# Kernel tuning notes

Measured on AMD Instinct MI355X. Metric: run time of the kernel, lower is better.

## Reference

```python
import jax, jax.numpy as jnp
import numpy as np

D_MODEL = 192
D_INNER = 384          # expand(2) * d_model
HEADDIM = 12
NHEADS = 32            # d_inner // headdim
DSTATE = 16
NGROUPS = 1
CONV_DIM = D_INNER + 2 * NGROUPS * DSTATE          # 416
D_IN_PROJ = 2 * D_INNER + 2 * NGROUPS * DSTATE + NHEADS  # 832
LN_EPS = 1e-5


def silu(x):
    return x * jax.nn.sigmoid(x)


def depthwise_conv2d(x_nchw, w, b):
    # groups == channels depthwise conv, kernel 3, padding 1 (SAME)
    out = jax.lax.conv_general_dilated(
        x_nchw, w, window_strides=(1, 1), padding='SAME',
        feature_group_count=CONV_DIM,
        dimension_numbers=('NCHW', 'OIHW', 'NCHW'))
    return out + b[None, :, None, None]


def setup_inputs() -> dict:
    key = jax.random.key(0)
    ks = jax.random.split(key, 10)
    Bn, H, W = 4, 128, 128
    u = jax.random.normal(ks[0], (Bn, H, W, D_MODEL), jnp.float32)
    t = jax.random.normal(ks[1], (Bn, H, W, D_MODEL), jnp.float32)
    s_in = 1.0 / np.sqrt(D_MODEL)
    W_in = jax.random.normal(ks[2], (D_IN_PROJ, D_MODEL), jnp.float32) * s_in
    W_t_in = jax.random.normal(ks[3], (D_IN_PROJ, D_MODEL), jnp.float32) * s_in
    conv_w = jax.random.normal(ks[4], (CONV_DIM, 1, 3, 3), jnp.float32) * (1.0 / 3.0)
    conv_b = jnp.zeros((CONV_DIM,), jnp.float32)
    # dt_bias = inverse-softplus of dt sampled log-uniform in [dt_min, dt_max]
    dt0 = jnp.exp(jax.random.uniform(ks[5], (NHEADS,)) * (np.log(0.1) - np.log(0.001)) + np.log(0.001))
    dt_bias = dt0 + jnp.log(-jnp.expm1(-dt0))
    A_log = jnp.log(jax.random.uniform(ks[6], (NHEADS,), minval=1.0, maxval=16.0))
    D = jnp.ones((NHEADS,), jnp.float32)
    ln_gamma = jnp.ones((D_INNER,), jnp.float32)
    ln_beta = jnp.zeros((D_INNER,), jnp.float32)
    W_out = jax.random.normal(ks[7], (D_MODEL, D_INNER), jnp.float32) * (1.0 / np.sqrt(D_INNER))
    return dict(u=u, t=t, W_in=W_in, W_t_in=W_t_in, conv_w=conv_w, conv_b=conv_b,
                dt_bias=dt_bias, A_log=A_log, D=D, ln_gamma=ln_gamma, ln_beta=ln_beta,
                W_out=W_out)


def reference(u, t, W_in, W_t_in, conv_w, conv_b, dt_bias, A_log, D,
              ln_gamma, ln_beta, W_out):
    B0, H, W_, C0 = u.shape
    L = H * W_
    uu = u.reshape(B0, L, C0)
    tt = t.reshape(B0, L, C0)

    # in_proj on main branch: split into z, xBC, dt
    zxbcdt = uu @ W_in.T                                    # (B, L, 832)
    z = zxbcdt[..., :D_INNER]                               # (B, L, 384)
    xBC = zxbcdt[..., D_INNER:D_INNER + CONV_DIM]           # (B, L, 416)
    dt = zxbcdt[..., D_INNER + CONV_DIM:]                   # (B, L, 32)
    dt = jax.nn.softplus(dt + dt_bias)

    # t branch: only x1B1C1 part is ultimately used (C := C1)
    x1B1C1 = (tt @ W_t_in.T)[..., D_INNER:D_INNER + CONV_DIM]

    # depthwise 3x3 conv + silu on both branches
    xBC = xBC.reshape(B0, H, W_, CONV_DIM).transpose(0, 3, 1, 2)
    xBC = silu(depthwise_conv2d(xBC, conv_w, conv_b))
    xBC = xBC.transpose(0, 2, 3, 1).reshape(B0, L, CONV_DIM)

    x1B1C1 = x1B1C1.reshape(B0, H, W_, CONV_DIM).transpose(0, 3, 1, 2)
    x1B1C1 = silu(depthwise_conv2d(x1B1C1, conv_w, conv_b))
    x1B1C1 = x1B1C1.transpose(0, 2, 3, 1).reshape(B0, L, CONV_DIM)

    x = xBC[..., :D_INNER]                                  # V features (B, L, 384)
    Bk = xBC[..., D_INNER:D_INNER + NGROUPS * DSTATE]       # K (B, L, 16)
    Cq = x1B1C1[..., D_INNER + NGROUPS * DSTATE:]           # Q from t-branch (B, L, 16)

    A = -jnp.exp(A_log)                                     # (nheads,), negative

    # non-causal linear attention duality (ngroups == 1)
    V = x.reshape(B0, L, NHEADS, HEADDIM).transpose(0, 2, 1, 3)   # (B, h, L, d)
    dtT = dt.transpose(0, 2, 1)                                   # (B, h, L)
    dA = -(dtT[..., None] * A[None, :, None, None])               # ssd_positve_dA: positive
    V_scaled = V * dA
    KV = jnp.einsum('bln,bhld->bhnd', Bk, V_scaled)               # (B, h, 16, 12)
    y = jnp.einsum('bln,bhnd->bhld', Cq, KV) + V * D[None, :, None, None]
    y = y.transpose(0, 2, 1, 3).reshape(B0, L, D_INNER)

    # LayerNorm over d_inner
    mu = jnp.mean(y, axis=-1, keepdims=True)
    var = jnp.mean((y - mu) ** 2, axis=-1, keepdims=True)
    y = (y - mu) * jax.lax.rsqrt(var + LN_EPS) * ln_gamma + ln_beta

    y = y * z
    out = y @ W_out.T
    return out.reshape(B0, H, W_, C0)
```

## Files before the change

### kernel.cpp

```cpp
#include <hip/hip_runtime.h>
#include <hip/hip_bf16.h>
#include <math.h>


#define BN 4
#define HH 128
#define WWID 128
#define LTOK (HH*WWID)
#define NTOK (BN*LTOK)
#define DMODEL 192
#define DINNER 384
#define NH 32
#define HD 12
#define DST 16
#define CONVD 416
#define KVCHUNKS 64
#define PM 256
#define TILE_SH 12288
#define TILE_BY 24576
#define TROW ((size_t)NTOK*64)
#define YPAD 392

typedef __hip_bfloat16 bf16;
typedef unsigned int uint32;
typedef unsigned short ushort16;
typedef __attribute__((ext_vector_type(8))) short bf16x8;
typedef __attribute__((ext_vector_type(4))) float f32x4;
typedef __attribute__((ext_vector_type(16))) float f32x16;

__device__ __forceinline__ float bflo(uint32 v){ return __uint_as_float((v & 0xffffu) << 16); }
__device__ __forceinline__ float bfhi(uint32 v){ return __uint_as_float(v & 0xffff0000u); }
__device__ __forceinline__ ushort16 f2bf(float f){
    __hip_bfloat16 h = __float2bfloat16(f);
    return *reinterpret_cast<const ushort16*>(&h);
}
__device__ __forceinline__ float ldbf(const bf16* p){
    return __uint_as_float(((uint32)(*(const ushort16*)p)) << 16);
}
__device__ __forceinline__ float ldbfs(const short* p){
    return __uint_as_float(((uint32)(ushort16)(*p)) << 16);
}
__device__ __forceinline__ float softplusf(float x){
    return (x > 20.f) ? x : log1pf(expf(x));
}
__device__ __forceinline__ float siluf(float x){
    return x / (1.f + expf(-x));
}

union BFPK { short s[8]; bf16x8 v; };

__global__ __launch_bounds__(256) void k_prep(
    const float* __restrict__ Win, const float* __restrict__ Wout,
    const float* __restrict__ cw,
    bf16* __restrict__ Wsw, bf16* __restrict__ Wout_sh, float* __restrict__ wtr)
{
    const int i = blockIdx.x*256 + threadIdx.x;
    if (i < 832*DMODEL) {
        const int ch = i / DMODEL, k = i - ch*DMODEL;
        const int nt = ch >> 6, row = ch & 63;
        const int ks = k ^ ((row & 7) << 3);
        Wsw[(size_t)nt*TILE_SH + row*DMODEL + ks] = __float2bfloat16(Win[i]);
    }
    if (i < DMODEL*DINNER) {
        const int m = i / DINNER, k = i - m*DINNER;
        const int ni = m >> 4, mr = m & 15;
        const int ks = k >> 5, kq = (k >> 3) & 3, ii = k & 7;
        const int lane = kq*16 + mr;
        Wout_sh[(size_t)((ni*12 + ks)*64 + lane)*8 + ii] = __float2bfloat16(Wout[i]);
    }
    if (i < CONVD*9) { const int c = i/9, k = i - c*9; wtr[k*420 + c] = cw[i]; }
}

__global__ __launch_bounds__(512) void k_proj_mfma(
    const float* __restrict__ u, const bf16* __restrict__ Wsw,
    const float* __restrict__ dt_b, const float* __restrict__ A_log,
    bf16* __restrict__ z_bf, bf16* __restrict__ xbc_pre, float* __restrict__ dA)
{
    __shared__ __align__(16) short S[3*TILE_SH];

    const int tid = threadIdx.x;
    const int m0 = blockIdx.x * PM;
    const int ntbase = blockIdx.y * 7;
    const int ntiles = blockIdx.y ? 6 : 7;
    const int wid = tid >> 6, lane = tid & 63;
    const int fr = lane & 31;
    const int hi = lane >> 5;

    const char* gW = (const char*)Wsw;
    auto GLOAD = [&](int nt, int buf) {
        const char* src = gW + (size_t)nt*TILE_BY + wid*3072 + lane*16;
        char* dst = ((char*)S) + buf*TILE_BY + wid*3072;
        #pragma unroll
        for (int c = 0; c < 3; ++c)
            __builtin_amdgcn_global_load_lds(
                (const __attribute__((address_space(1))) void*)(src + c*1024),
                (__attribute__((address_space(3))) void*)(dst + c*1024), 16, 0, 0);
    };

    GLOAD(ntbase, 0);

    const float db = dt_b[fr];
    const float al = expf(A_log[fr]);
    bf16x8 a[12];
    {
        const float* arow = u + (size_t)(m0 + wid*32 + fr)*DMODEL;
        #pragma unroll
        for (int ks=0;ks<12;++ks) {
            const float4 a0 = *(const float4*)(arow + ks*16 + hi*8);
            const float4 a1 = *(const float4*)(arow + ks*16 + hi*8 + 4);
            BFPK pk;
            pk.s[0]=(short)f2bf(a0.x); pk.s[1]=(short)f2bf(a0.y);
            pk.s[2]=(short)f2bf(a0.z); pk.s[3]=(short)f2bf(a0.w);
            pk.s[4]=(short)f2bf(a1.x); pk.s[5]=(short)f2bf(a1.y);
            pk.s[6]=(short)f2bf(a1.z); pk.s[7]=(short)f2bf(a1.w);
            a[ks] = pk.v;
        }
    }
    asm volatile("s_waitcnt vmcnt(0)" ::: "memory");
    GLOAD(ntbase + 1, 1);
    __builtin_amdgcn_s_barrier();
    __builtin_amdgcn_sched_barrier(0);

    const int kswz = (fr & 7) << 3;

    for (int i = 0; i < ntiles; ++i) {
        const int nt = ntbase + i;
        const short* Sb = &S[(i % 3)*TILE_SH];

        f32x16 acc0, acc1;
        #pragma unroll
        for (int q=0;q<16;++q) { acc0[q]=0.f; acc1[q]=0.f; }

        #pragma unroll
        for (int ks=0;ks<12;++ks) {
            const int kk = (ks*16 + hi*8) ^ kswz;
            const bf16x8 b0 = *(const bf16x8*)&Sb[fr*DMODEL + kk];
            const bf16x8 b1 = *(const bf16x8*)&Sb[(32+fr)*DMODEL + kk];
            acc0 = __builtin_amdgcn_mfma_f32_32x32x16_bf16(a[ks], b0, acc0, 0, 0, 0);
            acc1 = __builtin_amdgcn_mfma_f32_32x32x16_bf16(a[ks], b1, acc1, 0, 0, 0);
        }

        #pragma unroll
        for (int ni=0;ni<2;++ni) {
            const f32x16& ac = ni ? acc1 : acc0;
            const int n0 = nt*64 + ni*32;
            if (n0 < DINNER) {
                bf16* dst = z_bf + (size_t)nt*TROW + (ni*32 + fr);
                #pragma unroll
                for (int r=0;r<16;++r) {
                    const int tok = m0 + wid*32 + (r&3) + 8*(r>>2) + 4*hi;
                    dst[(size_t)tok*64] = __float2bfloat16(ac[r]);
                }
            } else if (n0 < 800) {
                const int loc = n0 - DINNER + fr;
                bf16* dst = xbc_pre + (size_t)(loc>>6)*TROW + (loc & 63);
                #pragma unroll
                for (int r=0;r<16;++r) {
                    const int tok = m0 + wid*32 + (r&3) + 8*(r>>2) + 4*hi;
                    dst[(size_t)tok*64] = __float2bfloat16(ac[r]);
                }
            } else {
                #pragma unroll
                for (int r=0;r<16;++r) {
                    const int tok = m0 + wid*32 + (r&3) + 8*(r>>2) + 4*hi;
                    const float dt = softplusf(ac[r] + db);
                    dA[(size_t)tok*NH + fr] = dt * al;
                }
            }
        }

        if (i + 2 < ntiles) {
            GLOAD(nt + 2, (i + 2) % 3);
            asm volatile("s_waitcnt vmcnt(35)" ::: "memory");
        } else {
            asm volatile("s_waitcnt vmcnt(32)" ::: "memory");
        }
        __builtin_amdgcn_s_barrier();
        __builtin_amdgcn_sched_barrier(0);
    }
}

__global__ __launch_bounds__(256) void k_tproj(
    const float* __restrict__ t, const float* __restrict__ Wtin, float* __restrict__ cq_pre)
{
    __shared__ float ts[16][196];
    __shared__ float ws[16][196];
    const int tid = threadIdx.x;
    const int tok0 = blockIdx.x * 16;
    #pragma unroll
    for (int i = 0; i < 3; ++i) {
        const int flat = tid + 256*i;
        const int row = flat / 48, c = (flat % 48)*4;
        *(float4*)&ts[row][c] = *(const float4*)(t    + (size_t)(tok0+row)*DMODEL + c);
        *(float4*)&ws[row][c] = *(const float4*)(Wtin + (size_t)(784+row)*DMODEL + c);
    }
    __syncthreads();
    const int tt = tid >> 4, n = tid & 15;
    float s0=0.f,s1=0.f,s2=0.f,s3=0.f;
    #pragma unroll 4
    for (int k = 0; k < DMODEL; k += 4) {
        s0 = fmaf(ts[tt][k+0], ws[n][k+0], s0);
        s1 = fmaf(ts[tt][k+1], ws[n][k+1], s1);
        s2 = fmaf(ts[tt][k+2], ws[n][k+2], s2);
        s3 = fmaf(ts[tt][k+3], ws[n][k+3], s3);
    }
    cq_pre[(size_t)(tok0+tt)*DST + n] = (s0+s1)+(s2+s3);
}

__global__ __launch_bounds__(416) void k_conv416(
    const bf16* __restrict__ in, const float* __restrict__ wtr, const float* __restrict__ cb,
    bf16* __restrict__ out)
{
    __shared__ float ws[9*420];
    __shared__ float bs[416];
    const int tid = threadIdx.x;
    for (int i = tid; i < 9*420; i += 416) ws[i] = wtr[i];
    if (tid < 416) bs[tid] = cb[tid];
    __syncthreads();

    const int pl  = tid / 52;
    const int grp = tid - pl*52;
    const int c0  = grp*8;
    const int pix = blockIdx.x*8 + pl;
    const int hw  = pix & (LTOK-1);
    const int h = hw >> 7, w = hw & 127;
    const int bb = pix >> 14;

    const bf16* inT = in + (size_t)(c0 >> 6)*TROW + (c0 & 63);

    float acc[8];
    {
        const float4 b0 = *(const float4*)&bs[c0];
        const float4 b1 = *(const float4*)&bs[c0+4];
        acc[0]=b0.x; acc[1]=b0.y; acc[2]=b0.z; acc[3]=b0.w;
        acc[4]=b1.x; acc[5]=b1.y; acc[6]=b1.z; acc[7]=b1.w;
    }

    #pragma unroll
    for (int dh=-1; dh<=1; ++dh) {
        const int hh = h + dh;
        if ((unsigned)hh >= (unsigned)HH) continue;
        #pragma unroll
        for (int dw=-1; dw<=1; ++dw) {
            const int w2 = w + dw;
            if ((unsigned)w2 >= (unsigned)WWID) continue;
            const int wi = (dh+1)*3 + (dw+1);
            const int pix2 = (bb<<14) + (hh<<7) + w2;
            const uint4 v = *(const uint4*)((const ushort16*)inT + (size_t)pix2*64);
            const float4 w0 = *(const float4*)&ws[wi*420 + c0];
            const float4 w1 = *(const float4*)&ws[wi*420 + c0 + 4];
            acc[0] = fmaf(bflo(v.x), w0.x, acc[0]);
            acc[1] = fmaf(bfhi(v.x), w0.y, acc[1]);
            acc[2] = fmaf(bflo(v.y), w0.z, acc[2]);
            acc[3] = fmaf(bfhi(v.y), w0.w, acc[3]);
            acc[4] = fmaf(bflo(v.z), w1.x, acc[4]);
            acc[5] = fmaf(bfhi(v.z), w1.y, acc[5]);
            acc[6] = fmaf(bflo(v.w), w1.z, acc[6]);
            acc[7] = fmaf(bfhi(v.w), w1.w, acc[7]);
        }
    }

    uint4 o;
    o.x = ((uint32)f2bf(siluf(acc[1])) << 16) | (uint32)f2bf(siluf(acc[0]));
    o.y = ((uint32)f2bf(siluf(acc[3])) << 16) | (uint32)f2bf(siluf(acc[2]));
    o.z = ((uint32)f2bf(siluf(acc[5])) << 16) | (uint32)f2bf(siluf(acc[4]));
    o.w = ((uint32)f2bf(siluf(acc[7])) << 16) | (uint32)f2bf(siluf(acc[6]));
    *(uint4*)((ushort16*)out + (size_t)pix*CONVD + c0) = o;
}

__global__ __launch_bounds__(256) void k_conv16(
    const float* __restrict__ in, const float* __restrict__ cw, const float* __restrict__ cb,
    bf16* __restrict__ out)
{
    const int idx = blockIdx.x*256 + threadIdx.x;
    const int cc = idx & 15;
    const int pix = idx >> 4;
    const int hw = pix & (LTOK-1);
    const int h = hw >> 7, w = hw & 127;
    const int bb = pix >> 14;
    const int c = 400 + cc;

    float wg[9];
    #pragma unroll
    for (int k=0;k<9;++k) wg[k] = cw[c*9+k];
    float a = cb[c];
    #pragma unroll
    for (int dh=-1; dh<=1; ++dh) {
        const int hh = h + dh;
        if ((unsigned)hh >= (unsigned)HH) continue;
        #pragma unroll
        for (int dw=-1; dw<=1; ++dw) {
            const int w2 = w + dw;
            if ((unsigned)w2 >= (unsigned)WWID) continue;
            a = fmaf(in[((size_t)((bb<<14)+(hh<<7)+w2))*16 + cc], wg[(dh+1)*3 + (dw+1)], a);
        }
    }
    out[(size_t)pix*16 + cc] = __float2bfloat16(siluf(a));
}

__global__ __launch_bounds__(512) void k_kv(
    const bf16* __restrict__ xbc_post, const float* __restrict__ dA,
    float* __restrict__ partial)
{
    __shared__ short vsb[16][408];
    __shared__ float das[16][32];
    const int tid = threadIdx.x;
    const int b = blockIdx.y;
    const int n = tid & 15;
    const int g = tid >> 4;

    float acc[12];
    #pragma unroll
    for (int j=0;j<12;++j) acc[j]=0.f;

    const int l0base = b*LTOK + blockIdx.x*256;

    for (int it = 0; it < 16; ++it) {
        const int l0 = l0base + it*16;
        for (int i = tid; i < 16*200; i += 512) {
            const int tok = i / 200;
            const int c2 = i - tok*200;
            const uint32 v = *(const uint32*)((const ushort16*)xbc_post
                                + (size_t)(l0+tok)*CONVD + c2*2);
            *(uint32*)&vsb[tok][c2*2] = v;
        }
        {
            const int tok = tid >> 5, h = tid & 31;
            das[tok][h] = dA[(size_t)(l0+tok)*NH + h];
        }
        __syncthreads();

        #pragma unroll
        for (int tok = 0; tok < 16; ++tok) {
            const uint32 bkraw = (uint32)(ushort16)vsb[tok][DINNER + n];
            const float s = __uint_as_float(bkraw << 16) * das[tok][g];
            const uint32* vp = (const uint32*)&vsb[tok][g*12];
            const uint32 w0 = vp[0], w1 = vp[1], w2 = vp[2];
            acc[0]  = fmaf(s, bflo(w0), acc[0]);
            acc[1]  = fmaf(s, bfhi(w0), acc[1]);
            acc[2]  = fmaf(s, bflo(w1), acc[2]);
            acc[3]  = fmaf(s, bfhi(w1), acc[3]);
            acc[4]  = fmaf(s, bflo(w2), acc[4]);
            acc[5]  = fmaf(s, bfhi(w2), acc[5]);
            const uint32* vq = (const uint32*)&vsb[tok][g*12 + 6];
            const uint32 w3 = vq[0], w4 = vq[1], w5 = vq[2];
            acc[6]  = fmaf(s, bflo(w3), acc[6]);
            acc[7]  = fmaf(s, bfhi(w3), acc[7]);
            acc[8]  = fmaf(s, bflo(w4), acc[8]);
            acc[9]  = fmaf(s, bfhi(w4), acc[9]);
            acc[10] = fmaf(s, bflo(w5), acc[10]);
            acc[11] = fmaf(s, bfhi(w5), acc[11]);
        }
        __syncthreads();
    }

    float* dst = partial + ((size_t)(b*KVCHUNKS + blockIdx.x))*6144 + (size_t)tid*12;
    #pragma unroll
    for (int j4=0;j4<3;++j4)
        *(float4*)(dst + j4*4) = make_float4(acc[j4*4], acc[j4*4+1], acc[j4*4+2], acc[j4*4+3]);
}

__global__ __launch_bounds__(256) void k_kvred(
    const float* __restrict__ partial, bf16* __restrict__ kvhl)
{
    const int idx = blockIdx.x*256 + threadIdx.x;
    const int b = idx / 6144;
    const int rem = idx - b*6144;
    const int hd = rem >> 4, n = rem & 15;
    const int h = hd / HD, d = hd - h*HD;
    const float* p = partial + (size_t)(b*KVCHUNKS)*6144 + h*192 + n*12 + d;
    float s = 0.f;
    #pragma unroll 4
    for (int c = 0; c < KVCHUNKS; ++c) s += p[(size_t)c*6144];
    const bf16 hi = __float2bfloat16(s);
    const float hif = ldbf(&hi);
    kvhl[((size_t)b*2 + 0)*6144 + rem] = hi;
    kvhl[((size_t)b*2 + 1)*6144 + rem] = __float2bfloat16(s - hif);
}

__global__ __launch_bounds__(256) void k_ynorm_out(
    const bf16* __restrict__ xbc_post, const bf16* __restrict__ cq_bf,
    const bf16* __restrict__ z_bf, const bf16* __restrict__ kvhl,
    const float* __restrict__ Dv, const float* __restrict__ ln_g, const float* __restrict__ ln_b,
    const bf16* __restrict__ Wout_sh, float* __restrict__ out)
{
    __shared__ __align__(16) short kvb[24*64*8];
    __shared__ __align__(16) short yzs[64*YPAD];
    __shared__ float gs[DINNER], bs2[DINNER], ds[DINNER];
    const int tid = threadIdx.x;
    const int token0 = blockIdx.x * 64;
    const int b = token0 >> 14;

    #pragma unroll
    for (int it = 0; it < 6; ++it) {
        const int f = tid + 256*it;
        const int t = f >> 6, l = f & 63;
        const int q = l >> 4;
        const short* src = (const short*)kvhl + ((size_t)b*2 + (q >> 1))*6144
                           + (t*16 + (l & 15))*16 + (q & 1)*8;
        *(uint4*)&kvb[(size_t)f*8] = *(const uint4*)src;
    }

    {
        const int row = tid >> 2, seg = tid & 3;
        const short* src = (const short*)xbc_post + (size_t)(token0+row)*CONVD + seg*96;
        short* dst = &yzs[row*YPAD + seg*96];
        #pragma unroll
        for (int j = 0; j < 12; ++j)
            *(uint4*)(dst + j*8) = *(const uint4*)(src + j*8);
    }

    for (int i = tid; i < DINNER; i += 256) {
        gs[i]  = ln_g[i];
        bs2[i] = ln_b[i];
        ds[i]  = Dv[i/HD];
    }
    __syncthreads();

    const int wid = tid >> 6, lane = tid & 63;
    const int fr = lane & 15, fq = lane >> 4;
    const int tokA = token0 + wid*16;

    const bf16x8 cqf = *(const bf16x8*)((const short*)cq_bf + (size_t)(tokA+fr)*DST + (fq&1)*8);

    f32x4 acc[24];
    #pragma unroll
    for (int t = 0; t < 24; ++t) {
        const bf16x8 bfv = *(const bf16x8*)&kvb[(t*64 + lane)*8];
        f32x4 z4 = (f32x4){0.f,0.f,0.f,0.f};
        acc[t] = __builtin_amdgcn_mfma_f32_16x16x32_bf16(cqf, bfv, z4, 0, 0, 0);
    }

    const int rloc0 = wid*16 + fq*4;
    const int tokj0 = tokA + fq*4;
    float s[4]  = {0.f,0.f,0.f,0.f};
    float s2[4] = {0.f,0.f,0.f,0.f};
    #pragma unroll
    for (int t = 0; t < 24; ++t) {
        const int hd = t*16 + fr;
        const float dvh = ds[hd];
        #pragma unroll
        for (int j = 0; j < 4; ++j) {
            const float vv = ldbfs(&yzs[(rloc0+j)*YPAD + hd]);
            const float y = fmaf(vv, dvh, acc[t][j]);
            acc[t][j] = y;
            s[j] += y;
            s2[j] = fmaf(y, y, s2[j]);
        }
    }
    #pragma unroll
    for (int j = 0; j < 4; ++j) {
        #pragma unroll
        for (int off = 8; off > 0; off >>= 1) {
            s[j]  += __shfl_xor(s[j],  off, 16);
            s2[j] += __shfl_xor(s2[j], off, 16);
        }
    }
    float mu[4], rs[4];
    #pragma unroll
    for (int j = 0; j < 4; ++j) {
        mu[j] = s[j] * (1.f/384.f);
        const float var = s2[j]*(1.f/384.f) - mu[j]*mu[j];
        rs[j] = rsqrtf(var + 1e-5f);
    }

    #pragma unroll
    for (int t = 0; t < 24; ++t) {
        const int hd = t*16 + fr;
        const float g = gs[hd], be = bs2[hd];
        const bf16* zsrc = z_bf + (size_t)(hd>>6)*TROW + (hd & 63);
        #pragma unroll
        for (int j = 0; j < 4; ++j) {
            const int tok = tokj0 + j;
            const float yn = fmaf((acc[t][j] - mu[j])*rs[j], g, be);
            const float zv = ldbf(zsrc + (size_t)tok*64);
            yzs[(rloc0+j)*YPAD + hd] = (short)f2bf(yn*zv);
        }
    }

    const short* yrow = &yzs[(wid*16 + fr)*YPAD];
    bf16x8 af[12];
    #pragma unroll
    for (int ks = 0; ks < 12; ++ks)
        af[ks] = *(const bf16x8*)(yrow + ks*32 + fq*8);

    f32x4 oacc[12];
    #pragma unroll
    for (int ni = 0; ni < 12; ++ni) oacc[ni] = (f32x4){0.f,0.f,0.f,0.f};

    #pragma unroll
    for (int ks = 0; ks < 12; ++ks) {
        #pragma unroll
        for (int ni = 0; ni < 12; ++ni) {
            const bf16x8 bw = *(const bf16x8*)((const short*)Wout_sh
                                + (size_t)((ni*12 + ks)*64 + lane)*8);
            oacc[ni] = __builtin_amdgcn_mfma_f32_16x16x32_bf16(af[ks], bw, oacc[ni], 0, 0, 0);
        }
    }

    #pragma unroll
    for (int ni = 0; ni < 12; ++ni) {
        const int n = ni*16 + fr;
        #pragma unroll
        for (int r = 0; r < 4; ++r)
            out[(size_t)(tokj0 + r)*DMODEL + n] = oacc[ni][r];
    }
}

extern "C" void kernel_launch(void* const* d_in, const int* in_sizes, int n_in,
                              void* d_out, int out_size, void* d_ws, size_t ws_size,
                              hipStream_t stream)
{
    const float* u      = (const float*)d_in[0];
    const float* t      = (const float*)d_in[1];
    const float* Win    = (const float*)d_in[2];
    const float* Wtin   = (const float*)d_in[3];
    const float* conv_w = (const float*)d_in[4];
    const float* conv_b = (const float*)d_in[5];
    const float* dt_b   = (const float*)d_in[6];
    const float* A_log  = (const float*)d_in[7];
    const float* Dv     = (const float*)d_in[8];
    const float* ln_g   = (const float*)d_in[9];
    const float* ln_bt  = (const float*)d_in[10];
    const float* W_out  = (const float*)d_in[11];
    float* out = (float*)d_out;

    char* p = (char*)d_ws;
    bf16* z_bf     = (bf16*)p;  p += (size_t)6*TROW*2;
    bf16* xbc_pre  = (bf16*)p;  p += (size_t)7*TROW*2;
    bf16* xbc_post = (bf16*)p;  p += (size_t)NTOK*CONVD*2;
    float* cq_pre  = (float*)p; p += (size_t)NTOK*DST*4;
    bf16* cq_bf    = (bf16*)p;  p += (size_t)NTOK*DST*2;
    float* dA      = (float*)p; p += (size_t)NTOK*NH*4;
    bf16* kvhl     = (bf16*)p;  p += (size_t)BN*2*6144*2;
    bf16* Wsw      = (bf16*)p;  p += (size_t)832*DMODEL*2;
    bf16* Wout_sh  = (bf16*)p;  p += (size_t)DMODEL*DINNER*2;
    float* wtr     = (float*)p; p += (size_t)9*420*4;

    float* kv_part = (float*)xbc_pre;

    k_prep<<<624, 256, 0, stream>>>(Win, W_out, conv_w, Wsw, Wout_sh, wtr);
    k_proj_mfma<<<dim3(NTOK/PM, 2), 512, 0, stream>>>(u, Wsw, dt_b, A_log, z_bf, xbc_pre, dA);
    k_tproj<<<NTOK/16, 256, 0, stream>>>(t, Wtin, cq_pre);
    k_conv416<<<NTOK/8, 416, 0, stream>>>(xbc_pre, wtr, conv_b, xbc_post);
    k_conv16<<<NTOK*16/256, 256, 0, stream>>>(cq_pre, conv_w, conv_b, cq_bf);
    k_kv<<<dim3(KVCHUNKS, BN), 512, 0, stream>>>(xbc_post, dA, kv_part);
    k_kvred<<<BN*6144/256, 256, 0, stream>>>(kv_part, kvhl);
    k_ynorm_out<<<NTOK/64, 256, 0, stream>>>(xbc_post, cq_bf, z_bf, kvhl,
                                             Dv, ln_g, ln_bt, Wout_sh, out);
}
```

Baseline: 295.6 us.

## Swap MFMA operands for row-contiguous vectorized epilogue stores and earlier prefetch

Swaps the A and B operands of the MFMAs in the input-projection and output-projection kernels, so each lane's accumulator registers hold consecutive output channels for a single token. The epilogues can then write packed 8-byte bf16 and 16-byte float4 stores instead of scattered 2-byte and 4-byte stores strided by token. The dt/A_log constants now come from per-channel vector loads inside the epilogue. The prefetch of tile i+2 is issued before the MFMA loop rather than after the epilogue, which changes the vmcnt wait count; this relies on the hand-tuned waitcnt matching the new number of outstanding loads.

```diff
diff --git a/kernel.cpp b/kernel.cpp
--- a/kernel.cpp
+++ b/kernel.cpp
@@ -48,6 +48,7 @@
 }
 
 union BFPK { short s[8]; bf16x8 v; };
+union BF4 { short s[4]; uint2 v; };
 
 __global__ __launch_bounds__(256) void k_prep(
     const float* __restrict__ Win, const float* __restrict__ Wout,
@@ -99,8 +100,6 @@
 
     GLOAD(ntbase, 0);
 
-    const float db = dt_b[fr];
-    const float al = expf(A_log[fr]);
     bf16x8 a[12];
     {
         const float* arow = u + (size_t)(m0 + wid*32 + fr)*DMODEL;
@@ -122,10 +121,13 @@
     __builtin_amdgcn_sched_barrier(0);
 
     const int kswz = (fr & 7) << 3;
+    const int tok = m0 + wid*32 + fr;
 
     for (int i = 0; i < ntiles; ++i) {
         const int nt = ntbase + i;
         const short* Sb = &S[(i % 3)*TILE_SH];
+
+        if (i + 2 < ntiles) GLOAD(nt + 2, (i + 2) % 3);
 
         f32x16 acc0, acc1;
         #pragma unroll
@@ -136,8 +138,8 @@
             const int kk = (ks*16 + hi*8) ^ kswz;
             const bf16x8 b0 = *(const bf16x8*)&Sb[fr*DMODEL + kk];
             const bf16x8 b1 = *(const bf16x8*)&Sb[(32+fr)*DMODEL + kk];
-            acc0 = __builtin_amdgcn_mfma_f32_32x32x16_bf16(a[ks], b0, acc0, 0, 0, 0);
-            acc1 = __builtin_amdgcn_mfma_f32_32x32x16_bf16(a[ks], b1, acc1, 0, 0, 0);
+            acc0 = __builtin_amdgcn_mfma_f32_32x32x16_bf16(b0, a[ks], acc0, 0, 0, 0);
+            acc1 = __builtin_amdgcn_mfma_f32_32x32x16_bf16(b1, a[ks], acc1, 0, 0, 0);
         }
 
         #pragma unroll
@@ -145,36 +147,42 @@
             const f32x16& ac = ni ? acc1 : acc0;
             const int n0 = nt*64 + ni*32;
             if (n0 < DINNER) {
-                bf16* dst = z_bf + (size_t)nt*TROW + (ni*32 + fr);
+                bf16* dst = z_bf + (size_t)nt*TROW + (size_t)tok*64 + ni*32 + 4*hi;
                 #pragma unroll
-                for (int r=0;r<16;++r) {
-                    const int tok = m0 + wid*32 + (r&3) + 8*(r>>2) + 4*hi;
-                    dst[(size_t)tok*64] = __float2bfloat16(ac[r]);
+                for (int q=0;q<4;++q) {
+                    BF4 pk;
+                    pk.s[0]=(short)f2bf(ac[q*4+0]); pk.s[1]=(short)f2bf(ac[q*4+1]);
+                    pk.s[2]=(short)f2bf(ac[q*4+2]); pk.s[3]=(short)f2bf(ac[q*4+3]);
+                    *(uint2*)((ushort16*)dst + q*8) = pk.v;
                 }
             } else if (n0 < 800) {
-                const int loc = n0 - DINNER + fr;
-                bf16* dst = xbc_pre + (size_t)(loc>>6)*TROW + (loc & 63);
+                const int loc = n0 - DINNER;
+                bf16* dst = xbc_pre + (size_t)(loc>>6)*TROW + (size_t)tok*64
+                            + (loc & 63) + 4*hi;
                 #pragma unroll
-                for (int r=0;r<16;++r) {
-                    const int tok = m0 + wid*32 + (r&3) + 8*(r>>2) + 4*hi;
-                    dst[(size_t)tok*64] = __float2bfloat16(ac[r]);
+                for (int q=0;q<4;++q) {
+                    BF4 pk;
+                    pk.s[0]=(short)f2bf(ac[q*4+0]); pk.s[1]=(short)f2bf(ac[q*4+1]);
+                    pk.s[2]=(short)f2bf(ac[q*4+2]); pk.s[3]=(short)f2bf(ac[q*4+3]);
+                    *(uint2*)((ushort16*)dst + q*8) = pk.v;
                 }
             } else {
+                float* dst = dA + (size_t)tok*NH + 4*hi;
                 #pragma unroll
-                for (int r=0;r<16;++r) {
-                    const int tok = m0 + wid*32 + (r&3) + 8*(r>>2) + 4*hi;
-                    const float dt = softplusf(ac[r] + db);
-                    dA[(size_t)tok*NH + fr] = dt * al;
+                for (int q=0;q<4;++q) {
+                    const float4 db4 = *(const float4*)(dt_b  + 8*q + 4*hi);
+                    const float4 al4 = *(const float4*)(A_log + 8*q + 4*hi);
+                    float4 o;
+                    o.x = softplusf(ac[q*4+0] + db4.x) * expf(al4.x);
+                    o.y = softplusf(ac[q*4+1] + db4.y) * expf(al4.y);
+                    o.z = softplusf(ac[q*4+2] + db4.z) * expf(al4.z);
+                    o.w = softplusf(ac[q*4+3] + db4.w) * expf(al4.w);
+                    *(float4*)(dst + q*8) = o;
                 }
             }
         }
 
-        if (i + 2 < ntiles) {
-            GLOAD(nt + 2, (i + 2) % 3);
-            asm volatile("s_waitcnt vmcnt(35)" ::: "memory");
-        } else {
-            asm volatile("s_waitcnt vmcnt(32)" ::: "memory");
-        }
+        asm volatile("s_waitcnt vmcnt(8)" ::: "memory");
         __builtin_amdgcn_s_barrier();
         __builtin_amdgcn_sched_barrier(0);
     }
@@ -494,16 +502,16 @@
         for (int ni = 0; ni < 12; ++ni) {
             const bf16x8 bw = *(const bf16x8*)((const short*)Wout_sh
                                 + (size_t)((ni*12 + ks)*64 + lane)*8);
-            oacc[ni] = __builtin_amdgcn_mfma_f32_16x16x32_bf16(af[ks], bw, oacc[ni], 0, 0, 0);
-        }
-    }
-
+            oacc[ni] = __builtin_amdgcn_mfma_f32_16x16x32_bf16(bw, af[ks], oacc[ni], 0, 0, 0);
+        }
+    }
+
+    float* orow = out + (size_t)(tokA + fr)*DMODEL + fq*4;
     #pragma unroll
     for (int ni = 0; ni < 12; ++ni) {
-        const int n = ni*16 + fr;
-        #pragma unroll
-        for (int r = 0; r < 4; ++r)
-            out[(size_t)(tokj0 + r)*DMODEL + n] = oacc[ni][r];
+        float4 o;
+        o.x = oacc[ni][0]; o.y = oacc[ni][1]; o.z = oacc[ni][2]; o.w = oacc[ni][3];
+        *(float4*)(orow + ni*16) = o;
     }
 }
 
```

After: 310.1 us. +4.9%, slower.
